# Kernel tuning notes

Hardware: AMD Instinct MI355X
Metric: run time of the kernel (lower is better)

Reference implementation:

```python
import jax, jax.numpy as jnp
import numpy as np

C = 512
CQK = C // 8   # 64
CV = C // 4    # 128

def setup_inputs() -> dict:
    key = jax.random.key(0)
    ks = jax.random.split(key, 10)
    B, H, W = 4, 64, 64
    s = 1.0 / np.sqrt(C)
    x = jax.random.normal(ks[0], (B, C, H, W), dtype=jnp.float32)
    Wq = jax.random.normal(ks[1], (CQK, C), dtype=jnp.float32) * s
    bq = jnp.zeros((CQK,), jnp.float32)
    Wk = jax.random.normal(ks[2], (CQK, C), dtype=jnp.float32) * s
    bk = jnp.zeros((CQK,), jnp.float32)
    Wv = jax.random.normal(ks[3], (CV, C), dtype=jnp.float32) * s
    bv = jnp.zeros((CV,), jnp.float32)
    Wo = jax.random.normal(ks[4], (C, CV), dtype=jnp.float32) * (1.0 / np.sqrt(CV))
    bo = jnp.zeros((C,), jnp.float32)
    gamma = jnp.ones((1,), jnp.float32) * 0.5  # nonzero so out path matters
    return {"x": x, "Wq": Wq, "bq": bq, "Wk": Wk, "bk": bk,
            "Wv": Wv, "bv": bv, "Wo": Wo, "bo": bo, "gamma": gamma}

def reference(x, Wq, bq, Wk, bk, Wv, bv, Wo, bo, gamma):
    B, C_, H, W = x.shape
    N = H * W
    xf = x.reshape(B, C_, N)                       # [B,C,N]
    # 1x1 convs == channel matmuls
    q = jnp.einsum('oc,bcn->bno', Wq, xf) + bq     # [B,N,Cqk]
    k = jnp.einsum('oc,bcn->bon', Wk, xf) + bk[None, :, None]  # [B,Cqk,N]
    v = jnp.einsum('oc,bcn->bon', Wv, xf) + bv[None, :, None]  # [B,Cv,N]
    attn = jax.nn.softmax(jnp.einsum('bno,bom->bnm', q, k), axis=-1)  # [B,N,N]
    out = jnp.einsum('bom,bnm->bon', v, attn)      # [B,Cv,N]
    out = jnp.einsum('oc,bcn->bon', Wo, out) + bo[None, :, None]  # [B,C,N]
    out = out.reshape(B, C_, H, W)
    return x + gamma * out
```

## Files before the change

kernel.cpp:

```cpp
#include <hip/hip_runtime.h>
#include <cstdint>
#include <cstddef>

#define N_SP 4096
#define C_IN 512
#define C_QK 64
#define C_V  128
#define LOG2E 1.4426950408889634f

typedef unsigned short u16;
typedef __attribute__((ext_vector_type(8))) short bf16x8;
typedef __attribute__((ext_vector_type(4))) float f32x4;
typedef __attribute__((ext_vector_type(16))) float f32x16;

__device__ __forceinline__ u16 f2bf(float f) {
    union { float f; uint32_t u; } x; x.f = f;
    const uint32_t r = x.u + 0x7fffu + ((x.u >> 16) & 1u);
    return (u16)(r >> 16);
}
__device__ __forceinline__ float bf2f(u16 b) {
    union { uint32_t u; float f; } x; x.u = ((uint32_t)b) << 16;
    return x.f;
}

__device__ __forceinline__ void* swzPtr(const void* base, int row, int colByte) {
    return (char*)base + row * 128 + (colByte ^ ((row & 7) << 4));
}

__global__ __launch_bounds__(256) void transpose_kernel(
    const float* __restrict__ x, u16* __restrict__ xb,
    const float* __restrict__ Wq, const float* __restrict__ Wk,
    const float* __restrict__ Wv, const float* __restrict__ Wo,
    u16* __restrict__ Wqb, u16* __restrict__ Wkb,
    u16* __restrict__ Wvb, u16* __restrict__ Wob)
{
    const int t = threadIdx.x;
    if (blockIdx.x >= 2048) {
        const int i = ((blockIdx.x - 2048) << 8) + t;
        const float* src; u16* dst; int off;
        if (i < 8192)       { src = Wq; dst = Wqb; off = i; }
        else if (i < 16384) { src = Wk; dst = Wkb; off = i - 8192; }
        else if (i < 32768) { src = Wv; dst = Wvb; off = i - 16384; }
        else                { src = Wo; dst = Wob; off = i - 32768; }
        const float4 v = *(const float4*)(src + ((size_t)off << 2));
        ushort4 h;
        h.x = f2bf(v.x); h.y = f2bf(v.y); h.z = f2bf(v.z); h.w = f2bf(v.w);
        *(ushort4*)(dst + ((size_t)off << 2)) = h;
        return;
    }
    __shared__ u16 ts[64 * 64];
    const int b  = blockIdx.x & 3;
    const int cc = (blockIdx.x >> 2) & 7;
    const int nc = blockIdx.x >> 5;
    const int c0 = cc << 6, n0 = nc << 6;
    const float* xs = x + ((size_t)(b * C_IN + c0) << 12) + n0;
    for (int u = t; u < 1024; u += 256) {
        const int c = u >> 4, nq = (u & 15) << 2;
        const float4 v = *(const float4*)(xs + ((size_t)c << 12) + nq);
        ushort4 h;
        h.x = f2bf(v.x); h.y = f2bf(v.y); h.z = f2bf(v.z); h.w = f2bf(v.w);
        *(ushort4*)((char*)ts + c * 128 + ((nq << 1) ^ (((c >> 3) & 7) << 4))) = h;
    }
    __syncthreads();
    for (int u = t; u < 512; u += 256) {
        const int n = u >> 3, cg = u & 7;
        u16 pk[8];
        #pragma unroll
        for (int j = 0; j < 8; ++j) {
            const int c = (cg << 3) + j;
            pk[j] = *(const u16*)((char*)ts + c * 128 + ((n << 1) ^ (cg << 4)));
        }
        *(ushort4*)(xb + ((size_t)((b << 12) + n0 + n) << 9) + c0 + (cg << 3)) =
            *(ushort4*)&pk[0];
        *(ushort4*)(xb + ((size_t)((b << 12) + n0 + n) << 9) + c0 + (cg << 3) + 4) =
            *(ushort4*)&pk[4];
    }
}

__global__ __launch_bounds__(256) void qkv_kernel(
    const u16* __restrict__ xb,
    const u16* __restrict__ Wqb, const float* __restrict__ bq,
    const u16* __restrict__ Wkb, const float* __restrict__ bk,
    const u16* __restrict__ Wvb, const float* __restrict__ bv,
    u16* __restrict__ Qb, u16* __restrict__ Kf, u16* __restrict__ Vf)
{
    __shared__ u16 wt[64 * 64];
    __shared__ u16 xt[64 * 64];
    const int t = threadIdx.x;
    const int l = t & 63, w = t >> 6;
    const int lo = l & 15, hi = l >> 4;
    const int b  = blockIdx.x & 3;
    const int ot = (blockIdx.x >> 2) & 3;
    const int n0 = (blockIdx.x >> 4) << 6;
    const u16* Wbase = (ot == 0) ? Wqb : (ot == 1) ? Wkb : (Wvb + ((ot - 2) << 6) * C_IN);
    f32x4 acc[4];
    #pragma unroll
    for (int ti = 0; ti < 4; ++ti) acc[ti] = (f32x4){0.f, 0.f, 0.f, 0.f};

    for (int cc = 0; cc < 8; ++cc) {
        const int c0 = cc << 6;
        for (int u = t; u < 512; u += 256) {
            const int i = u >> 3, cb = (u & 7) << 4;
            *(uint4*)swzPtr(wt, i, cb) =
                *(const uint4*)(Wbase + (size_t)i * C_IN + c0 + (cb >> 1));
        }
        for (int u = t; u < 512; u += 256) {
            const int i = u >> 3, cb = (u & 7) << 4;
            *(uint4*)swzPtr(xt, i, cb) =
                *(const uint4*)(xb + ((size_t)((b << 12) + n0 + i) << 9) + c0 + (cb >> 1));
        }
        __syncthreads();
        if (ot < 2) {
            const bf16x8 af0 = *(const bf16x8*)swzPtr(xt, (w << 4) + lo, hi << 4);
            const bf16x8 af1 = *(const bf16x8*)swzPtr(xt, (w << 4) + lo, 64 + (hi << 4));
            #pragma unroll
            for (int ti = 0; ti < 4; ++ti) {
                const bf16x8 bf0 = *(const bf16x8*)swzPtr(wt, (ti << 4) + lo, hi << 4);
                const bf16x8 bf1 = *(const bf16x8*)swzPtr(wt, (ti << 4) + lo, 64 + (hi << 4));
                acc[ti] = __builtin_amdgcn_mfma_f32_16x16x32_bf16(af0, bf0, acc[ti], 0, 0, 0);
                acc[ti] = __builtin_amdgcn_mfma_f32_16x16x32_bf16(af1, bf1, acc[ti], 0, 0, 0);
            }
        } else {
            const bf16x8 af0 = *(const bf16x8*)swzPtr(wt, (w << 4) + lo, hi << 4);
            const bf16x8 af1 = *(const bf16x8*)swzPtr(wt, (w << 4) + lo, 64 + (hi << 4));
            #pragma unroll
            for (int ti = 0; ti < 4; ++ti) {
                const bf16x8 bf0 = *(const bf16x8*)swzPtr(xt, (ti << 4) + lo, hi << 4);
                const bf16x8 bf1 = *(const bf16x8*)swzPtr(xt, (ti << 4) + lo, 64 + (hi << 4));
                acc[ti] = __builtin_amdgcn_mfma_f32_16x16x32_bf16(af0, bf0, acc[ti], 0, 0, 0);
                acc[ti] = __builtin_amdgcn_mfma_f32_16x16x32_bf16(af1, bf1, acc[ti], 0, 0, 0);
            }
        }
        __syncthreads();
    }
    const int kt = n0 >> 6;
    if (ot == 0) {
        #pragma unroll
        for (int ti = 0; ti < 4; ++ti) {
            const float bias = bq[(ti << 4) + lo];
            #pragma unroll
            for (int r = 0; r < 4; ++r) {
                const int nrow = (w << 4) + (hi << 2) + r;
                Qb[((size_t)((b << 12) + n0 + nrow) << 6) + (ti << 4) + lo] =
                    f2bf((acc[ti][r] + bias) * LOG2E);
            }
        }
    } else if (ot == 1) {
        #pragma unroll
        for (int ti = 0; ti < 4; ++ti) {
            const int ch = (ti << 4) + lo;
            const float bias = bk[ch];
            #pragma unroll
            for (int r = 0; r < 4; ++r) {
                const int key = (w << 4) + (hi << 2) + r;
                const int sid = (ti << 1) + (key >> 5);
                const int lpos = (((ch >> 3) & 1) << 5) + (key & 31);
                Kf[(((size_t)((b << 6) + kt) << 3) + sid) * 512 + (lpos << 3) + (ch & 7)] =
                    f2bf(acc[ti][r] + bias);
            }
        }
    } else {
        #pragma unroll
        for (int r = 0; r < 4; ++r) {
            const int cv = ((ot - 2) << 6) + (w << 4) + (hi << 2) + r;
            const float bias = bv[cv];
            #pragma unroll
            for (int ti = 0; ti < 4; ++ti) {
                const int nl = (ti << 4) + lo;
                const int sv = ((cv >> 5) << 2) + ti;
                const int lpos = (((nl >> 3) & 1) << 5) + (cv & 31);
                Vf[(((size_t)((b << 6) + kt) << 4) + sv) * 512 + (lpos << 3) + (nl & 7)] =
                    f2bf(acc[ti][r] + bias);
            }
        }
    }
}


#define KLOAD(dst, ktl)                                                        \
    {                                                                          \
        const size_t o_ = ((size_t)(((s << 4) + ((ktl) & 15)) << 3)) * 512;    \
        _Pragma("unroll")                                                      \
        for (int i_ = 0; i_ < 8; ++i_)                                         \
            dst[i_] = *(const bf16x8*)(kfb + o_ + i_ * 512);                   \
    }

#define VLOAD(dst, ktl, tjIdx)                                                 \
    {                                                                          \
        const size_t o_ = ((size_t)(((s << 4) + ((ktl) & 15)) << 4) + ((tjIdx) << 2)) * 512; \
        _Pragma("unroll")                                                      \
        for (int i_ = 0; i_ < 4; ++i_)                                         \
            dst[i_] = *(const bf16x8*)(vfb + o_ + i_ * 512);                   \
    }

#define TILE(kt, kfU, kfP)                                                    \
    {                                                                         \
        bf16x8 vA[4], vB[4], vC[4];                                           \
        VLOAD(vA, kt, 0);                                                     \
        f32x16 sa0, sa1;                                                      \
        _Pragma("unroll")                                                     \
        for (int i = 0; i < 16; ++i) { sa0[i] = 0.f; sa1[i] = 0.f; }          \
        __builtin_amdgcn_s_setprio(1);                                        \
        _Pragma("unroll")                                                     \
        for (int ks = 0; ks < 4; ++ks) {                                      \
            sa0 = __builtin_amdgcn_mfma_f32_32x32x16_bf16(kfU[(ks << 1)], qf[ks], sa0, 0, 0, 0);     \
            sa1 = __builtin_amdgcn_mfma_f32_32x32x16_bf16(kfU[(ks << 1) + 1], qf[ks], sa1, 0, 0, 0); \
        }                                                                     \
        __builtin_amdgcn_s_setprio(0);                                        \
        KLOAD(kfP, (kt) + 1);                                                 \
        VLOAD(vB, kt, 1);                                                     \
        float p0[16], p1[16];                                                 \
        _Pragma("unroll")                                                     \
        for (int i = 0; i < 16; ++i) {                                        \
            p0[i] = exp2f(sa0[i]);                                            \
            p1[i] = exp2f(sa1[i]);                                            \
        }                                                                     \
        float sm8[8];                                                         \
        _Pragma("unroll")                                                     \
        for (int i = 0; i < 8; ++i) sm8[i] = (p0[i] + p0[i + 8]) + (p1[i] + p1[i + 8]); \
        _Pragma("unroll")                                                     \
        for (int i = 0; i < 4; ++i) sm8[i] += sm8[i + 4];                     \
        lsum += (sm8[0] + sm8[1]) + (sm8[2] + sm8[3]);                        \
        VLOAD(vC, kt, 2);                                                     \
        uint32_t P2[2][4][2];                                                 \
        _Pragma("unroll")                                                     \
        for (int g = 0; g < 4; ++g) {                                         \
            _Pragma("unroll")                                                 \
            for (int pr = 0; pr < 2; ++pr) {                                  \
                asm("v_cvt_pk_bf16_f32 %0, %1, %2"                            \
                    : "=v"(P2[0][g][pr]) : "v"(p0[4 * g + 2 * pr]), "v"(p0[4 * g + 2 * pr + 1])); \
                asm("v_cvt_pk_bf16_f32 %0, %1, %2"                            \
                    : "=v"(P2[1][g][pr]) : "v"(p1[4 * g + 2 * pr]), "v"(p1[4 * g + 2 * pr + 1])); \
            }                                                                 \
        }                                                                     \
        bf16x8 pf[4];                                                         \
        _Pragma("unroll")                                                     \
        for (int ks = 0; ks < 4; ++ks) {                                      \
            const int iE = ks << 1, iO = iE + 1;                              \
            uint32_t fr[4];                                                   \
            _Pragma("unroll")                                                 \
            for (int pr = 0; pr < 2; ++pr) {                                  \
                uint32_t X = P2[iE >> 2][iE & 3][pr];                         \
                uint32_t Y = P2[iO >> 2][iO & 3][pr];                         \
                asm("v_permlane32_swap_b32 %0, %1" : "+v"(X), "+v"(Y));       \
                fr[pr]     = X;                            \
                fr[2 + pr] = Y;                            \
            }                                                                 \
            pf[ks] = *(bf16x8*)fr;                                            \
        }                                                                     \
        __builtin_amdgcn_s_setprio(1);                                        \
        _Pragma("unroll")                                                     \
        for (int ks = 0; ks < 4; ++ks)                                        \
            oacc[0] = __builtin_amdgcn_mfma_f32_32x32x16_bf16(vA[ks], pf[ks], oacc[0], 0, 0, 0); \
        __builtin_amdgcn_s_setprio(0);                                        \
        VLOAD(vA, kt, 3);                                                     \
        __builtin_amdgcn_s_setprio(1);                                        \
        _Pragma("unroll")                                                     \
        for (int ks = 0; ks < 4; ++ks)                                        \
            oacc[1] = __builtin_amdgcn_mfma_f32_32x32x16_bf16(vB[ks], pf[ks], oacc[1], 0, 0, 0); \
        _Pragma("unroll")                                                     \
        for (int ks = 0; ks < 4; ++ks)                                        \
            oacc[2] = __builtin_amdgcn_mfma_f32_32x32x16_bf16(vC[ks], pf[ks], oacc[2], 0, 0, 0); \
        _Pragma("unroll")                                                     \
        for (int ks = 0; ks < 4; ++ks)                                        \
            oacc[3] = __builtin_amdgcn_mfma_f32_32x32x16_bf16(vA[ks], pf[ks], oacc[3], 0, 0, 0); \
        __builtin_amdgcn_s_setprio(0);                                        \
    }

__global__ __launch_bounds__(256, 2) void attn_kernel(
    const u16* __restrict__ Qb, const u16* __restrict__ Kf,
    const u16* __restrict__ Vf, u16* __restrict__ po,
    float* __restrict__ pl)
{
    const int t = threadIdx.x;
    const int l = t & 63, w = t >> 6;
    const int l31 = l & 31, h = l >> 5;
    const int b = blockIdx.x & 3;
    const int s = (blockIdx.x >> 2) & 3;
    const int qc = blockIdx.x >> 4;
    const int n0 = qc << 7;
    const int kt0 = ((blockIdx.x >> 8) & 1) << 3;

    const u16* qp = Qb + ((size_t)((b << 12) + n0 + (w << 5) + l31) << 6) + (h << 3);
    bf16x8 qf[4];
    #pragma unroll
    for (int ks = 0; ks < 4; ++ks) qf[ks] = *(const bf16x8*)(qp + (ks << 4));

    const u16* kfb = Kf + (((size_t)(b << 6)) << 12) + (l << 3);
    const u16* vfb = Vf + (((size_t)(b << 6)) << 13) + (l << 3);

    float lsum = 0.f;
    f32x16 oacc[4];
    #pragma unroll
    for (int tj = 0; tj < 4; ++tj)
        #pragma unroll
        for (int i = 0; i < 16; ++i) oacc[tj][i] = 0.f;

    bf16x8 kfA[8], kfB[8];
    KLOAD(kfA, kt0);

    for (int kk = 0; kk < 16; kk += 2) {
        TILE(kt0 + kk, kfA, kfB);
        TILE(kt0 + kk + 1, kfB, kfA);
    }

    lsum += __shfl_xor(lsum, 32);
    u16* pod = po + ((size_t)blockIdx.x << 14);
    #pragma unroll
    for (int tj = 0; tj < 4; ++tj)
        #pragma unroll
        for (int r = 0; r < 16; ++r) {
            const int cv = (tj << 5) + (r & 3) + ((r >> 2) << 3) + (h << 2);
            pod[(cv << 7) + (w << 5) + l31] = f2bf(oacc[tj][r]);
        }
    if (h == 0) pl[(blockIdx.x << 7) + (w << 5) + l31] = lsum;
}

__global__ __launch_bounds__(256) void combine_kernel(
    const u16* __restrict__ po, const float* __restrict__ pl,
    u16* __restrict__ Ob)
{
    __shared__ float invl[64];
    __shared__ float tr[64][132];
    const int t = threadIdx.x;
    const int b = blockIdx.x & 3;
    const int qh = (blockIdx.x >> 2) & 1;
    const int qc = blockIdx.x >> 3;
    int slot[4];
    #pragma unroll
    for (int s = 0; s < 4; ++s) slot[s] = b + (s << 2) + (qc << 4);
    if (t < 64) {
        const int q = (qh << 6) + t;
        float lg = 0.f;
        #pragma unroll
        for (int s = 0; s < 4; ++s) lg += pl[(slot[s] << 7) + q];
        invl[t] = 1.0f / lg;
    }
    __syncthreads();
    for (int u = t; u < 2048; u += 256) {
        const int cv = u >> 4, q4 = (u & 15) << 2;
        const int q = (qh << 6) + q4;
        float a0 = 0.f, a1 = 0.f, a2 = 0.f, a3 = 0.f;
        #pragma unroll
        for (int s = 0; s < 4; ++s) {
            const ushort4 hv =
                *(const ushort4*)(po + ((size_t)slot[s] << 14) + (cv << 7) + q);
            a0 += bf2f(hv.x); a1 += bf2f(hv.y);
            a2 += bf2f(hv.z); a3 += bf2f(hv.w);
        }
        tr[q4 + 0][cv] = a0 * invl[q4 + 0];
        tr[q4 + 1][cv] = a1 * invl[q4 + 1];
        tr[q4 + 2][cv] = a2 * invl[q4 + 2];
        tr[q4 + 3][cv] = a3 * invl[q4 + 3];
    }
    __syncthreads();
    for (int u = t; u < 2048; u += 256) {
        const int q = u >> 5, c4 = (u & 31) << 2;
        const float4 v = *(const float4*)&tr[q][c4];
        ushort4 o;
        o.x = f2bf(v.x); o.y = f2bf(v.y); o.z = f2bf(v.z); o.w = f2bf(v.w);
        const int n = (qc << 7) + (qh << 6) + q;
        *(ushort4*)(Ob + ((size_t)((b << 12) + n) << 7) + c4) = o;
    }
}

__global__ __launch_bounds__(256) void proj_kernel(
    const u16* __restrict__ Ob, const u16* __restrict__ Wob,
    const float* __restrict__ bo, const float* __restrict__ x,
    const float* __restrict__ gamma_p, float* __restrict__ out)
{
    __shared__ union {
        struct { u16 wl0[64 * 64]; u16 wl1[64 * 64]; u16 ob0[64 * 64]; u16 ob1[64 * 64]; } s;
        float tr[64 * 64];
    } sm;
    const int t = threadIdx.x;
    const int l = t & 63, w = t >> 6;
    const int lo = l & 15, hi = l >> 4;
    const int b  = blockIdx.x & 3;
    const int co0 = ((blockIdx.x >> 2) & 7) << 6;
    const int n0  = (blockIdx.x >> 5) << 6;
    for (int u = t; u < 1024; u += 256) {
        const int i = u >> 4, cb = (u & 15) << 4;
        *(uint4*)swzPtr((cb < 128) ? sm.s.wl0 : sm.s.wl1, i, cb & 127) =
            *(const uint4*)(Wob + (size_t)(co0 + i) * C_V + (cb >> 1));
    }
    for (int u = t; u < 1024; u += 256) {
        const int i = u >> 4, cb = (u & 15) << 4;
        *(uint4*)swzPtr((cb < 128) ? sm.s.ob0 : sm.s.ob1, i, cb & 127) =
            *(const uint4*)(Ob + ((size_t)((b << 12) + n0 + i) << 7) + (cb >> 1));
    }
    __syncthreads();
    const int arow = (w << 4) + lo;
    const bf16x8 af00 = *(const bf16x8*)swzPtr(sm.s.wl0, arow, hi << 4);
    const bf16x8 af01 = *(const bf16x8*)swzPtr(sm.s.wl0, arow, 64 + (hi << 4));
    const bf16x8 af10 = *(const bf16x8*)swzPtr(sm.s.wl1, arow, hi << 4);
    const bf16x8 af11 = *(const bf16x8*)swzPtr(sm.s.wl1, arow, 64 + (hi << 4));
    f32x4 acc[4];
    #pragma unroll
    for (int ti = 0; ti < 4; ++ti) {
        const int brow = (ti << 4) + lo;
        f32x4 z = (f32x4){0.f, 0.f, 0.f, 0.f};
        z = __builtin_amdgcn_mfma_f32_16x16x32_bf16(af00, *(const bf16x8*)swzPtr(sm.s.ob0, brow, hi << 4), z, 0, 0, 0);
        z = __builtin_amdgcn_mfma_f32_16x16x32_bf16(af01, *(const bf16x8*)swzPtr(sm.s.ob0, brow, 64 + (hi << 4)), z, 0, 0, 0);
        z = __builtin_amdgcn_mfma_f32_16x16x32_bf16(af10, *(const bf16x8*)swzPtr(sm.s.ob1, brow, hi << 4), z, 0, 0, 0);
        acc[ti] = __builtin_amdgcn_mfma_f32_16x16x32_bf16(af11, *(const bf16x8*)swzPtr(sm.s.ob1, brow, 64 + (hi << 4)), z, 0, 0, 0);
    }
    __syncthreads();
    #pragma unroll
    for (int ti = 0; ti < 4; ++ti)
        #pragma unroll
        for (int r = 0; r < 4; ++r) {
            const int co = (w << 4) + (hi << 2) + r;
            const int n  = (ti << 4) + lo;
            sm.tr[(co << 6) + (n ^ (((co >> 2) & 3) << 2))] = acc[ti][r];
        }
    __syncthreads();
    const float g = gamma_p[0];
    for (int u = t; u < 1024; u += 256) {
        const int co = u >> 4, n4 = (u & 15) << 2;
        const float4 av = *(const float4*)&sm.tr[(co << 6) + (n4 ^ (((co >> 2) & 3) << 2))];
        const int o = co0 + co;
        const size_t off = ((size_t)(b * C_IN + o) << 12) + n0 + n4;
        const float4 xv = *(const float4*)(x + off);
        const float bias = bo[o];
        float4 rs;
        rs.x = xv.x + g * (av.x + bias);
        rs.y = xv.y + g * (av.y + bias);
        rs.z = xv.z + g * (av.z + bias);
        rs.w = xv.w + g * (av.w + bias);
        *(float4*)(out + off) = rs;
    }
}

extern "C" void kernel_launch(void* const* d_in, const int* in_sizes, int n_in,
                              void* d_out, int out_size, void* d_ws, size_t ws_size,
                              hipStream_t stream) {
    (void)in_sizes; (void)n_in; (void)out_size; (void)ws_size;
    const float* x  = (const float*)d_in[0];
    const float* Wq = (const float*)d_in[1];
    const float* bq = (const float*)d_in[2];
    const float* Wk = (const float*)d_in[3];
    const float* bk = (const float*)d_in[4];
    const float* Wv = (const float*)d_in[5];
    const float* bv = (const float*)d_in[6];
    const float* Wo = (const float*)d_in[7];
    const float* bo = (const float*)d_in[8];
    const float* gm = (const float*)d_in[9];
    float* out = (float*)d_out;
    u16* xb = (u16*)d_ws;
    u16* po = (u16*)d_ws;
    u16* Qb = (u16*)((char*)d_ws + ((size_t)16 << 20));
    u16* Kf = Qb + (size_t)4 * N_SP * C_QK;
    u16* Vf = Kf + (size_t)4 * N_SP * C_QK;
    float* pl = (float*)((char*)d_ws + ((size_t)24 << 20));
    u16* Ob = (u16*)((char*)d_ws + ((size_t)24 << 20) + (256 << 10));
    u16* Wqb = (u16*)((char*)d_ws + ((size_t)24 << 20) + (256 << 10) + ((size_t)4 << 20));
    u16* Wkb = Wqb + 64 * 512;
    u16* Wvb = Wkb + 64 * 512;
    u16* Wob = Wvb + 128 * 512;
    transpose_kernel<<<2240, 256, 0, stream>>>(x, xb, Wq, Wk, Wv, Wo,
                                               Wqb, Wkb, Wvb, Wob);
    qkv_kernel<<<1024, 256, 0, stream>>>(xb, Wqb, bq, Wkb, bk, Wvb, bv, Qb, Kf, Vf);
    attn_kernel<<<512, 256, 0, stream>>>(Qb, Kf, Vf, po, pl);
    combine_kernel<<<256, 256, 0, stream>>>(po, pl, Ob);
    proj_kernel<<<2048, 256, 0, stream>>>(Ob, Wob, bo, x, gm, out);
}
```

Before: 96.30 us.

## Stage K/V tiles through double-buffered LDS via global_load_lds shared by waves

Previously each wave loaded the K and V fragments for every key tile straight from global memory into registers, duplicating the loads across the four waves of a block. The new code cooperatively copies each key tile's K and V slices into double-buffered shared memory with global_load_lds (6 loads per wave), waits on vmcnt and barriers, then all waves read fragments from LDS. This cuts redundant global/L2 traffic and register pressure. In exchange it adds two block barriers per tile, about 48KB of LDS that may limit occupancy, and LDS read latency on the MFMA path. The per-block kt0 offset is also dropped, so every block now starts its key loop at tile 0 rather than staggering.

Measured after the change: 99.65 us. 3.5% more time.

```diff
diff --git a/kernel.cpp b/kernel.cpp
--- a/kernel.cpp
+++ b/kernel.cpp
@@ -25,6 +25,12 @@
 
 __device__ __forceinline__ void* swzPtr(const void* base, int row, int colByte) {
     return (char*)base + row * 128 + (colByte ^ ((row & 7) << 4));
+}
+
+__device__ __forceinline__ void gl16(const u16* g, u16* l) {
+    __builtin_amdgcn_global_load_lds(
+        (const __attribute__((address_space(1))) void*)g,
+        (__attribute__((address_space(3))) void*)l, 16, 0, 0);
 }
 
 __global__ __launch_bounds__(256) void transpose_kernel(
@@ -177,38 +183,37 @@
 }
 
 
-#define KLOAD(dst, ktl)                                                        \
+#define CFENCE asm volatile("" ::: "memory")
+
+#define STAGE(bufi, ktg)                                                       \
     {                                                                          \
-        const size_t o_ = ((size_t)(((s << 4) + ((ktl) & 15)) << 3)) * 512;    \
+        const int kta_ = (s << 4) + ((ktg) & 15);                              \
         _Pragma("unroll")                                                      \
-        for (int i_ = 0; i_ < 8; ++i_)                                         \
-            dst[i_] = *(const bf16x8*)(kfb + o_ + i_ * 512);                   \
-    }
-
-#define VLOAD(dst, ktl, tjIdx)                                                 \
-    {                                                                          \
-        const size_t o_ = ((size_t)(((s << 4) + ((ktl) & 15)) << 4) + ((tjIdx) << 2)) * 512; \
-        _Pragma("unroll")                                                      \
-        for (int i_ = 0; i_ < 4; ++i_)                                         \
-            dst[i_] = *(const bf16x8*)(vfb + o_ + i_ * 512);                   \
-    }
-
-#define TILE(kt, kfU, kfP)                                                    \
+        for (int i_ = 0; i_ < 6; ++i_) {                                       \
+            const int sid_ = w * 6 + i_;                                       \
+            if (sid_ < 8)                                                      \
+                gl16(kfbL + (((size_t)kta_ << 3) + sid_) * 512 + (l << 3),     \
+                     &ksm[bufi][sid_ * 512]);                                  \
+            else                                                               \
+                gl16(vfbL + (((size_t)kta_ << 4) + (sid_ - 8)) * 512 + (l << 3),\
+                     &vsm[bufi][(sid_ - 8) * 512]);                            \
+        }                                                                      \
+    }
+
+#define TILE(cur)                                                             \
     {                                                                         \
-        bf16x8 vA[4], vB[4], vC[4];                                           \
-        VLOAD(vA, kt, 0);                                                     \
         f32x16 sa0, sa1;                                                      \
         _Pragma("unroll")                                                     \
         for (int i = 0; i < 16; ++i) { sa0[i] = 0.f; sa1[i] = 0.f; }          \
         __builtin_amdgcn_s_setprio(1);                                        \
         _Pragma("unroll")                                                     \
         for (int ks = 0; ks < 4; ++ks) {                                      \
-            sa0 = __builtin_amdgcn_mfma_f32_32x32x16_bf16(kfU[(ks << 1)], qf[ks], sa0, 0, 0, 0);     \
-            sa1 = __builtin_amdgcn_mfma_f32_32x32x16_bf16(kfU[(ks << 1) + 1], qf[ks], sa1, 0, 0, 0); \
+            const bf16x8 k0 = *(const bf16x8*)(&ksm[cur][((ks << 1)) * 512] + (l << 3));      \
+            const bf16x8 k1 = *(const bf16x8*)(&ksm[cur][((ks << 1) + 1) * 512] + (l << 3));  \
+            sa0 = __builtin_amdgcn_mfma_f32_32x32x16_bf16(k0, qf[ks], sa0, 0, 0, 0);          \
+            sa1 = __builtin_amdgcn_mfma_f32_32x32x16_bf16(k1, qf[ks], sa1, 0, 0, 0);          \
         }                                                                     \
         __builtin_amdgcn_s_setprio(0);                                        \
-        KLOAD(kfP, (kt) + 1);                                                 \
-        VLOAD(vB, kt, 1);                                                     \
         float p0[16], p1[16];                                                 \
         _Pragma("unroll")                                                     \
         for (int i = 0; i < 16; ++i) {                                        \
@@ -221,7 +226,6 @@
         _Pragma("unroll")                                                     \
         for (int i = 0; i < 4; ++i) sm8[i] += sm8[i + 4];                     \
         lsum += (sm8[0] + sm8[1]) + (sm8[2] + sm8[3]);                        \
-        VLOAD(vC, kt, 2);                                                     \
         uint32_t P2[2][4][2];                                                 \
         _Pragma("unroll")                                                     \
         for (int g = 0; g < 4; ++g) {                                         \
@@ -243,27 +247,20 @@
                 uint32_t X = P2[iE >> 2][iE & 3][pr];                         \
                 uint32_t Y = P2[iO >> 2][iO & 3][pr];                         \
                 asm("v_permlane32_swap_b32 %0, %1" : "+v"(X), "+v"(Y));       \
-                fr[pr]     = X;                            \
-                fr[2 + pr] = Y;                            \
+                fr[pr]     = X;                                               \
+                fr[2 + pr] = Y;                                               \
             }                                                                 \
             pf[ks] = *(bf16x8*)fr;                                            \
         }                                                                     \
         __builtin_amdgcn_s_setprio(1);                                        \
         _Pragma("unroll")                                                     \
-        for (int ks = 0; ks < 4; ++ks)                                        \
-            oacc[0] = __builtin_amdgcn_mfma_f32_32x32x16_bf16(vA[ks], pf[ks], oacc[0], 0, 0, 0); \
-        __builtin_amdgcn_s_setprio(0);                                        \
-        VLOAD(vA, kt, 3);                                                     \
-        __builtin_amdgcn_s_setprio(1);                                        \
-        _Pragma("unroll")                                                     \
-        for (int ks = 0; ks < 4; ++ks)                                        \
-            oacc[1] = __builtin_amdgcn_mfma_f32_32x32x16_bf16(vB[ks], pf[ks], oacc[1], 0, 0, 0); \
-        _Pragma("unroll")                                                     \
-        for (int ks = 0; ks < 4; ++ks)                                        \
-            oacc[2] = __builtin_amdgcn_mfma_f32_32x32x16_bf16(vC[ks], pf[ks], oacc[2], 0, 0, 0); \
-        _Pragma("unroll")                                                     \
-        for (int ks = 0; ks < 4; ++ks)                                        \
-            oacc[3] = __builtin_amdgcn_mfma_f32_32x32x16_bf16(vA[ks], pf[ks], oacc[3], 0, 0, 0); \
+        for (int tj = 0; tj < 4; ++tj)                                        \
+            _Pragma("unroll")                                                 \
+            for (int ks = 0; ks < 4; ++ks) {                                  \
+                const bf16x8 vf =                                             \
+                    *(const bf16x8*)(&vsm[cur][((tj << 2) + ks) * 512] + (l << 3)); \
+                oacc[tj] = __builtin_amdgcn_mfma_f32_32x32x16_bf16(vf, pf[ks], oacc[tj], 0, 0, 0); \
+            }                                                                 \
         __builtin_amdgcn_s_setprio(0);                                        \
     }
 
@@ -272,6 +269,8 @@
     const u16* __restrict__ Vf, u16* __restrict__ po,
     float* __restrict__ pl)
 {
+    __shared__ u16 ksm[2][8 * 512];
+    __shared__ u16 vsm[2][16 * 512];
     const int t = threadIdx.x;
     const int l = t & 63, w = t >> 6;
     const int l31 = l & 31, h = l >> 5;
@@ -279,15 +278,14 @@
     const int s = (blockIdx.x >> 2) & 3;
     const int qc = blockIdx.x >> 4;
     const int n0 = qc << 7;
-    const int kt0 = ((blockIdx.x >> 8) & 1) << 3;
 
     const u16* qp = Qb + ((size_t)((b << 12) + n0 + (w << 5) + l31) << 6) + (h << 3);
     bf16x8 qf[4];
     #pragma unroll
     for (int ks = 0; ks < 4; ++ks) qf[ks] = *(const bf16x8*)(qp + (ks << 4));
 
-    const u16* kfb = Kf + (((size_t)(b << 6)) << 12) + (l << 3);
-    const u16* vfb = Vf + (((size_t)(b << 6)) << 13) + (l << 3);
+    const u16* kfbL = Kf + (((size_t)(b << 6)) << 12);
+    const u16* vfbL = Vf + (((size_t)(b << 6)) << 13);
 
     float lsum = 0.f;
     f32x16 oacc[4];
@@ -296,12 +294,20 @@
         #pragma unroll
         for (int i = 0; i < 16; ++i) oacc[tj][i] = 0.f;
 
-    bf16x8 kfA[8], kfB[8];
-    KLOAD(kfA, kt0);
-
-    for (int kk = 0; kk < 16; kk += 2) {
-        TILE(kt0 + kk, kfA, kfB);
-        TILE(kt0 + kk + 1, kfB, kfA);
+    STAGE(0, 0);
+    for (int tt = 0; tt < 16; ++tt) {
+        const int cur = tt & 1;
+        if (tt < 15) {
+            STAGE(cur ^ 1, tt + 1);
+            asm volatile("s_waitcnt vmcnt(6)" ::: "memory");
+        } else {
+            asm volatile("s_waitcnt vmcnt(0)" ::: "memory");
+        }
+        __builtin_amdgcn_s_barrier();
+        CFENCE;
+        if (cur == 0) { TILE(0); } else { TILE(1); }
+        CFENCE;
+        __builtin_amdgcn_s_barrier();
     }
 
     lsum += __shfl_xor(lsum, 32);
```
